# Kernel tuning notes

Hardware: AMD Instinct MI355X
Metric: run time of the kernel (lower is better)

Reference implementation:

```python
import jax, jax.numpy as jnp
import numpy as np

H = 256
T = 2048
B = 64


def setup_inputs() -> dict:
    key = jax.random.key(0)
    ks = jax.random.split(key, 10)
    s = 1.0 / np.sqrt(H)
    return {
        "x": jax.random.normal(ks[0], (T, B, H), dtype=jnp.float32),
        # AttentionLayer params
        "W_b": jax.random.normal(ks[1], (H, H), dtype=jnp.float32) * s,
        "b_b": jnp.zeros((H,), dtype=jnp.float32),
        "v_b": jax.random.normal(ks[2], (1, H), dtype=jnp.float32) * s,
        "W_e": jax.random.normal(ks[3], (H, 2 * H), dtype=jnp.float32) * s,
        "b_e": jnp.zeros((H,), dtype=jnp.float32),
        # LSTMCell params (PyTorch layout: [4H, H], gate order i,f,g,o)
        "W_ih": jax.random.uniform(ks[4], (4 * H, H), dtype=jnp.float32, minval=-s, maxval=s),
        "W_hh": jax.random.uniform(ks[5], (4 * H, H), dtype=jnp.float32, minval=-s, maxval=s),
        "b_ih": jax.random.uniform(ks[6], (4 * H,), dtype=jnp.float32, minval=-s, maxval=s),
        "b_hh": jax.random.uniform(ks[7], (4 * H,), dtype=jnp.float32, minval=-s, maxval=s),
    }


def reference(x, W_b, b_b, v_b, W_e, b_e, W_ih, W_hh, b_ih, b_hh):
    # x: [T, B, H]. Effective recurrence per timestep (inner per-sample loop in
    # the original is dead code: its output writes are overwritten and its
    # states start from zeros each iteration).
    def step(carry, xi):
        h, c = carry  # [B, H] each
        hc = jnp.concatenate([h, c], axis=1)  # [B, 2H]
        a = hc @ W_e.T + b_e                  # [B, H]
        b = xi @ W_b.T + b_b                  # [B, H]
        j = jnp.tanh(a + b) @ v_b.T           # [B, 1]
        w = jax.nn.softmax(j, axis=0) * xi    # softmax over batch dim, [B, H]
        gates = w @ W_ih.T + b_ih + h @ W_hh.T + b_hh  # [B, 4H]
        i_g, f_g, g_g, o_g = jnp.split(gates, 4, axis=1)
        c_new = jax.nn.sigmoid(f_g) * c + jax.nn.sigmoid(i_g) * jnp.tanh(g_g)
        h_new = jax.nn.sigmoid(o_g) * jnp.tanh(c_new)
        return (h_new, c_new), h_new

    Bn, Hn = x.shape[1], x.shape[2]
    init = (jnp.zeros((Bn, Hn), x.dtype), jnp.zeros((Bn, Hn), x.dtype))
    _, output = jax.lax.scan(step, init, x)  # [T, B, H]
    return output
```

## Files before the change

kernel.cpp:

```cpp
#include <hip/hip_runtime.h>
#include <math.h>

constexpr int H   = 256;
constexpr int B   = 64;
constexpr int T   = 2048;
constexpr int G   = 64;
constexpr int NTH = 512;
constexpr int HB  = H * B;

struct SharedMain {
    float wU[256][16];
    float wV[256][16];
    float wA[768][4];
    float U[64][17];
    float V[64][17];
    float ap[64][5];
    alignas(16) float outst[64][4];
    float jp[8][64];
    float bg[16];
    float ba[4];
    float v4[4];
    float s[64];
};
union SharedAll {
    SharedMain m;
    float tile[64][65];
};

__device__ __forceinline__ float sigmoidf_(float v) {
    return 1.0f / (1.0f + expf(-v));
}

__device__ __forceinline__ void grid_barrier(unsigned* bar, unsigned target) {
    __syncthreads();
    if (threadIdx.x == 0) {
        __threadfence();
        __hip_atomic_fetch_add(bar, 1u, __ATOMIC_ACQ_REL, __HIP_MEMORY_SCOPE_AGENT);
        while (__hip_atomic_load(bar, __ATOMIC_ACQUIRE, __HIP_MEMORY_SCOPE_AGENT) < target) {
            __builtin_amdgcn_s_sleep(1);
        }
        __threadfence();
    }
    __syncthreads();
}

__global__ void __launch_bounds__(NTH, 1)
scan_kernel(const float* __restrict__ x,
            const float* __restrict__ W_b,  const float* __restrict__ b_b,
            const float* __restrict__ v_b,  const float* __restrict__ W_e,
            const float* __restrict__ b_e,  const float* __restrict__ W_ih,
            const float* __restrict__ W_hh, const float* __restrict__ b_ih,
            const float* __restrict__ b_hh,
            float* __restrict__ out, float* __restrict__ wsf,
            unsigned* __restrict__ bar)
{
    __shared__ SharedAll sh;
    const int tid = threadIdx.x;
    const int g   = blockIdx.x;

    float* pJ = wsf + 64;
    float* hT = pJ + G * 64;
    float* cT = hT + HB;
    float* xT = out;

    for (int tl = g; tl < T * 4; tl += G) {
        const int t  = tl >> 2;
        const int kc = (tl & 3) << 6;
        __syncthreads();
        for (int q = tid; q < 1024; q += NTH) {
            const int r  = q >> 4;
            const int c4 = (q & 15) << 2;
            const float4 v = *(const float4*)(x + (size_t)t * HB + (size_t)r * H + kc + c4);
            sh.tile[r][c4 + 0] = v.x; sh.tile[r][c4 + 1] = v.y;
            sh.tile[r][c4 + 2] = v.z; sh.tile[r][c4 + 3] = v.w;
        }
        __syncthreads();
        for (int q = tid; q < 1024; q += NTH) {
            const int k  = q >> 4;
            const int b4 = (q & 15) << 2;
            float4 v;
            v.x = sh.tile[b4 + 0][k]; v.y = sh.tile[b4 + 1][k];
            v.z = sh.tile[b4 + 2][k]; v.w = sh.tile[b4 + 3][k];
            *(float4*)(xT + (size_t)t * HB + (size_t)(kc + k) * B + b4) = v;
        }
    }
    __syncthreads();

    for (int e = tid; e < 256 * 16; e += NTH) {
        const int k  = e >> 4;
        const int cl = e & 15;
        const int gate = cl >> 2, oi = cl & 3;
        const int row = gate * H + 4 * g + oi;
        sh.m.wU[k][cl] = W_ih[(size_t)row * H + k];
        sh.m.wV[k][cl] = W_hh[(size_t)row * H + k];
    }
    for (int e = tid; e < 768 * 4; e += NTH) {
        const int r = e >> 2;
        const int i = e & 3;
        const int col = 4 * g + i;
        float w;
        if (r < 512) w = W_e[(size_t)col * 512 + r];
        else         w = W_b[(size_t)col * 256 + (r - 512)];
        sh.m.wA[r][i] = w;
    }
    if (tid < 16) {
        const int gate = tid >> 2, oi = tid & 3;
        const int col = gate * H + 4 * g + oi;
        sh.m.bg[tid] = b_ih[col] + b_hh[col];
    }
    if (tid < 4) {
        sh.m.ba[tid] = b_e[4 * g + tid] + b_b[4 * g + tid];
        sh.m.v4[tid] = v_b[4 * g + tid];
    }
    hT[g * NTH + tid] = 0.0f;

    unsigned nb = 0;
    ++nb; grid_barrier(bar, nb * (unsigned)G);

    const int wv = tid >> 6;
    const int b  = tid & 63;

    for (int t = 0; t < T; ++t) {
        for (int e = tid; e < 64 * 17; e += NTH) { (&sh.m.U[0][0])[e] = 0.0f; (&sh.m.V[0][0])[e] = 0.0f; }
        for (int e = tid; e < 64 * 5; e += NTH) (&sh.m.ap[0][0])[e] = 0.0f;
        __syncthreads();

        if (wv < 4) {
            const int krow = wv << 6;
            const float* src = xT + (size_t)t * HB + (size_t)krow * B;
            float aU[16], aA[4];
            #pragma unroll
            for (int c = 0; c < 16; ++c) aU[c] = 0.0f;
            aA[0] = aA[1] = aA[2] = aA[3] = 0.0f;
            #pragma unroll 4
            for (int kk = 0; kk < 64; ++kk) {
                const float xv = src[kk * B + b];
                const float* wr = sh.m.wU[krow + kk];
                #pragma unroll
                for (int c = 0; c < 16; ++c) aU[c] = fmaf(xv, wr[c], aU[c]);
                const float* wa = sh.m.wA[512 + krow + kk];
                #pragma unroll
                for (int i = 0; i < 4; ++i) aA[i] = fmaf(xv, wa[i], aA[i]);
            }
            #pragma unroll
            for (int c = 0; c < 16; ++c) atomicAdd(&sh.m.U[b][c], aU[c]);
            #pragma unroll
            for (int i = 0; i < 4; ++i) atomicAdd(&sh.m.ap[b][i], aA[i]);
        } else {
            const int krow = (wv - 4) << 6;
            const float* sH = hT + (size_t)krow * B;
            const float* sC = cT + (size_t)krow * B;
            float aV[16], aA[4];
            #pragma unroll
            for (int c = 0; c < 16; ++c) aV[c] = 0.0f;
            aA[0] = aA[1] = aA[2] = aA[3] = 0.0f;
            #pragma unroll 4
            for (int kk = 0; kk < 64; ++kk) {
                const float hv = sH[kk * B + b];
                const float cv = sC[kk * B + b];
                const float* wr = sh.m.wV[krow + kk];
                #pragma unroll
                for (int c = 0; c < 16; ++c) aV[c] = fmaf(hv, wr[c], aV[c]);
                const float* waH = sh.m.wA[krow + kk];
                const float* waC = sh.m.wA[256 + krow + kk];
                #pragma unroll
                for (int i = 0; i < 4; ++i) aA[i] = fmaf(hv, waH[i], fmaf(cv, waC[i], aA[i]));
            }
            #pragma unroll
            for (int c = 0; c < 16; ++c) atomicAdd(&sh.m.V[b][c], aV[c]);
            #pragma unroll
            for (int i = 0; i < 4; ++i) atomicAdd(&sh.m.ap[b][i], aA[i]);
        }
        __syncthreads();

        if (tid < 64) {
            float pj = 0.0f;
            #pragma unroll
            for (int i = 0; i < 4; ++i)
                pj += tanhf(sh.m.ap[tid][i] + sh.m.ba[i]) * sh.m.v4[i];
            pJ[g * 64 + tid] = pj;
        }
        ++nb; grid_barrier(bar, nb * (unsigned)G);

        {
            float jpart = 0.0f;
            const int base = wv * 8;
            #pragma unroll
            for (int gg = 0; gg < 8; ++gg) jpart += pJ[(base + gg) * 64 + b];
            sh.m.jp[wv][b] = jpart;
        }
        __syncthreads();
        if (tid < 64) {
            float jv = 0.0f;
            #pragma unroll
            for (int w = 0; w < 8; ++w) jv += sh.m.jp[w][tid];
            float mx = jv;
            #pragma unroll
            for (int off = 32; off; off >>= 1) mx = fmaxf(mx, __shfl_xor(mx, off));
            const float e = expf(jv - mx);
            float ssum = e;
            #pragma unroll
            for (int off = 32; off; off >>= 1) ssum += __shfl_xor(ssum, off);
            sh.m.s[tid] = e / ssum;
        }
        __syncthreads();

        if (tid < 256) {
            const int oi = tid >> 6;
            const int bb = tid & 63;
            const float sb = sh.m.s[bb];
            const float pI = fmaf(sb, sh.m.U[bb][0  + oi], sh.m.V[bb][0  + oi]) + sh.m.bg[0  + oi];
            const float pF = fmaf(sb, sh.m.U[bb][4  + oi], sh.m.V[bb][4  + oi]) + sh.m.bg[4  + oi];
            const float pG = fmaf(sb, sh.m.U[bb][8  + oi], sh.m.V[bb][8  + oi]) + sh.m.bg[8  + oi];
            const float pO = fmaf(sb, sh.m.U[bb][12 + oi], sh.m.V[bb][12 + oi]) + sh.m.bg[12 + oi];
            const int col = 4 * g + oi;
            const float cold = cT[col * B + bb];
            const float cnew = sigmoidf_(pF) * cold + sigmoidf_(pI) * tanhf(pG);
            const float hnew = sigmoidf_(pO) * tanhf(cnew);
            cT[col * B + bb] = cnew;
            hT[col * B + bb] = hnew;
            sh.m.outst[bb][oi] = hnew;
        }
        __syncthreads();
        if (tid < 64) {
            const float4 v = *(const float4*)sh.m.outst[tid];
            *(float4*)(out + (size_t)t * HB + (size_t)tid * H + 4 * g) = v;
        }
        ++nb; grid_barrier(bar, nb * (unsigned)G);
    }
}

extern "C" void kernel_launch(void* const* d_in, const int* in_sizes, int n_in,
                              void* d_out, int out_size, void* d_ws, size_t ws_size,
                              hipStream_t stream) {
    const float* x    = (const float*)d_in[0];
    const float* W_b  = (const float*)d_in[1];
    const float* b_b  = (const float*)d_in[2];
    const float* v_b  = (const float*)d_in[3];
    const float* W_e  = (const float*)d_in[4];
    const float* b_e  = (const float*)d_in[5];
    const float* W_ih = (const float*)d_in[6];
    const float* W_hh = (const float*)d_in[7];
    const float* b_ih = (const float*)d_in[8];
    const float* b_hh = (const float*)d_in[9];
    float*    out = (float*)d_out;
    float*    wsf = (float*)d_ws;
    unsigned* bar = (unsigned*)d_ws;

    hipMemsetAsync(d_ws, 0, 256, stream);

    void* args[] = { &x, &W_b, &b_b, &v_b, &W_e, &b_e, &W_ih, &W_hh, &b_ih, &b_hh,
                     &out, &wsf, &bar };
    hipLaunchCooperativeKernel((void*)scan_kernel, dim3(G), dim3(NTH), args, 0, stream);
}
```

Baseline: 89.99 ms.

## Replace grid barriers with split arrive/wait counters and double-buffered partials

Replaces the two full grid barriers per timestep with separate arrive/wait counters: one for the attention-score partials, which are now double-buffered by step parity, and one for h/c readiness. The h/c wait is deferred until after each block's x-projection, so that independent work overlaps other blocks' progress. Both the x-projection and the h/c-projection phases are now spread over all 8 waves instead of 4 each. Barrier fences are relaxed to explicit release/acquire fences. The aim is to cut the grid-synchronisation latency that dominates this latency-bound recurrence, at the cost of more delicate memory-ordering reasoning.

```diff
diff --git a/kernel.cpp b/kernel.cpp
--- a/kernel.cpp
+++ b/kernel.cpp
@@ -7,6 +7,7 @@
 constexpr int G   = 64;
 constexpr int NTH = 512;
 constexpr int HB  = H * B;
+constexpr int W   = 2;
 
 struct SharedMain {
     float wU[256][16];
@@ -31,17 +32,17 @@
     return 1.0f / (1.0f + expf(-v));
 }
 
-__device__ __forceinline__ void grid_barrier(unsigned* bar, unsigned target) {
-    __syncthreads();
-    if (threadIdx.x == 0) {
-        __threadfence();
-        __hip_atomic_fetch_add(bar, 1u, __ATOMIC_ACQ_REL, __HIP_MEMORY_SCOPE_AGENT);
-        while (__hip_atomic_load(bar, __ATOMIC_ACQUIRE, __HIP_MEMORY_SCOPE_AGENT) < target) {
-            __builtin_amdgcn_s_sleep(1);
-        }
-        __threadfence();
-    }
-    __syncthreads();
+__device__ __forceinline__ void fence_rel() { __builtin_amdgcn_fence(__ATOMIC_RELEASE, "agent"); }
+__device__ __forceinline__ void fence_acq() { __builtin_amdgcn_fence(__ATOMIC_ACQUIRE, "agent"); }
+
+__device__ __forceinline__ void arrive(unsigned* c) {
+    fence_rel();
+    __hip_atomic_fetch_add(c, 1u, __ATOMIC_RELAXED, __HIP_MEMORY_SCOPE_AGENT);
+}
+__device__ __forceinline__ void wait_for(unsigned* c, unsigned target) {
+    while (__hip_atomic_load(c, __ATOMIC_RELAXED, __HIP_MEMORY_SCOPE_AGENT) < target)
+        __builtin_amdgcn_s_sleep(1);
+    fence_acq();
 }
 
 __global__ void __launch_bounds__(NTH, 1)
@@ -51,15 +52,21 @@
             const float* __restrict__ b_e,  const float* __restrict__ W_ih,
             const float* __restrict__ W_hh, const float* __restrict__ b_ih,
             const float* __restrict__ b_hh,
-            float* __restrict__ out, float* __restrict__ wsf,
-            unsigned* __restrict__ bar)
+            float* __restrict__ out, float* __restrict__ wsf)
 {
     __shared__ SharedAll sh;
     const int tid = threadIdx.x;
     const int g   = blockIdx.x;
 
-    float* pJ = wsf + 64;
-    float* hT = pJ + G * 64;
+    unsigned* cnt = (unsigned*)wsf;
+    unsigned* bar = cnt + 0;
+    unsigned* dj0 = cnt + 16;
+    unsigned* dj1 = cnt + 32;
+    unsigned* dh0 = cnt + 48;
+    unsigned* dh1 = cnt + 64;
+
+    float* pJ = wsf + 128;
+    float* hT = pJ + W * G * 64;
     float* cT = hT + HB;
     float* xT = out;
 
@@ -114,31 +121,37 @@
     }
     hT[g * NTH + tid] = 0.0f;
 
-    unsigned nb = 0;
-    ++nb; grid_barrier(bar, nb * (unsigned)G);
+    __threadfence_block();
+    __syncthreads();
+    if (tid == 0) { arrive(bar); wait_for(bar, (unsigned)G); }
+    __syncthreads();
 
     const int wv = tid >> 6;
     const int b  = tid & 63;
 
     for (int t = 0; t < T; ++t) {
+        const int slot = t & 1;
+        unsigned* dj = slot ? dj1 : dj0;
+        const unsigned tgt = (unsigned)G * ((unsigned)(t >> 1) + 1u);
+
         for (int e = tid; e < 64 * 17; e += NTH) { (&sh.m.U[0][0])[e] = 0.0f; (&sh.m.V[0][0])[e] = 0.0f; }
         for (int e = tid; e < 64 * 5; e += NTH) (&sh.m.ap[0][0])[e] = 0.0f;
         __syncthreads();
 
-        if (wv < 4) {
-            const int krow = wv << 6;
-            const float* src = xT + (size_t)t * HB + (size_t)krow * B;
+        {
+            const int kw = wv << 5;
+            const float* src = xT + (size_t)t * HB + (size_t)kw * B;
             float aU[16], aA[4];
             #pragma unroll
             for (int c = 0; c < 16; ++c) aU[c] = 0.0f;
             aA[0] = aA[1] = aA[2] = aA[3] = 0.0f;
             #pragma unroll 4
-            for (int kk = 0; kk < 64; ++kk) {
+            for (int kk = 0; kk < 32; ++kk) {
                 const float xv = src[kk * B + b];
-                const float* wr = sh.m.wU[krow + kk];
+                const float* wr = sh.m.wU[kw + kk];
                 #pragma unroll
                 for (int c = 0; c < 16; ++c) aU[c] = fmaf(xv, wr[c], aU[c]);
-                const float* wa = sh.m.wA[512 + krow + kk];
+                const float* wa = sh.m.wA[512 + kw + kk];
                 #pragma unroll
                 for (int i = 0; i < 4; ++i) aA[i] = fmaf(xv, wa[i], aA[i]);
             }
@@ -146,23 +159,31 @@
             for (int c = 0; c < 16; ++c) atomicAdd(&sh.m.U[b][c], aU[c]);
             #pragma unroll
             for (int i = 0; i < 4; ++i) atomicAdd(&sh.m.ap[b][i], aA[i]);
-        } else {
-            const int krow = (wv - 4) << 6;
-            const float* sH = hT + (size_t)krow * B;
-            const float* sC = cT + (size_t)krow * B;
+        }
+
+        if (tid == 0 && t > 0) {
+            unsigned* dh = ((t - 1) & 1) ? dh1 : dh0;
+            wait_for(dh, (unsigned)G * ((unsigned)((t - 1) >> 1) + 1u));
+        }
+        __syncthreads();
+
+        {
+            const int kw = wv << 5;
+            const float* sH = hT + (size_t)kw * B;
+            const float* sC = cT + (size_t)kw * B;
             float aV[16], aA[4];
             #pragma unroll
             for (int c = 0; c < 16; ++c) aV[c] = 0.0f;
             aA[0] = aA[1] = aA[2] = aA[3] = 0.0f;
             #pragma unroll 4
-            for (int kk = 0; kk < 64; ++kk) {
+            for (int kk = 0; kk < 32; ++kk) {
                 const float hv = sH[kk * B + b];
                 const float cv = sC[kk * B + b];
-                const float* wr = sh.m.wV[krow + kk];
+                const float* wr = sh.m.wV[kw + kk];
                 #pragma unroll
                 for (int c = 0; c < 16; ++c) aV[c] = fmaf(hv, wr[c], aV[c]);
-                const float* waH = sh.m.wA[krow + kk];
-                const float* waC = sh.m.wA[256 + krow + kk];
+                const float* waH = sh.m.wA[kw + kk];
+                const float* waC = sh.m.wA[256 + kw + kk];
                 #pragma unroll
                 for (int i = 0; i < 4; ++i) aA[i] = fmaf(hv, waH[i], fmaf(cv, waC[i], aA[i]));
             }
@@ -178,15 +199,19 @@
             #pragma unroll
             for (int i = 0; i < 4; ++i)
                 pj += tanhf(sh.m.ap[tid][i] + sh.m.ba[i]) * sh.m.v4[i];
-            pJ[g * 64 + tid] = pj;
-        }
-        ++nb; grid_barrier(bar, nb * (unsigned)G);
+            pJ[(size_t)slot * G * 64 + g * 64 + tid] = pj;
+            __threadfence_block();
+        }
+        __syncthreads();
+        if (tid == 0) { arrive(dj); wait_for(dj, tgt); }
+        __syncthreads();
 
         {
             float jpart = 0.0f;
             const int base = wv * 8;
-            #pragma unroll
-            for (int gg = 0; gg < 8; ++gg) jpart += pJ[(base + gg) * 64 + b];
+            const float* pjs = pJ + (size_t)slot * G * 64;
+            #pragma unroll
+            for (int gg = 0; gg < 8; ++gg) jpart += pjs[(base + gg) * 64 + b];
             sh.m.jp[wv][b] = jpart;
         }
         __syncthreads();
@@ -220,13 +245,15 @@
             cT[col * B + bb] = cnew;
             hT[col * B + bb] = hnew;
             sh.m.outst[bb][oi] = hnew;
-        }
-        __syncthreads();
+            __threadfence_block();
+        }
+        __syncthreads();
+        if (tid == 0) arrive(slot ? dh1 : dh0);
+
         if (tid < 64) {
             const float4 v = *(const float4*)sh.m.outst[tid];
             *(float4*)(out + (size_t)t * HB + (size_t)tid * H + 4 * g) = v;
         }
-        ++nb; grid_barrier(bar, nb * (unsigned)G);
     }
 }
 
@@ -245,11 +272,10 @@
     const float* b_hh = (const float*)d_in[9];
     float*    out = (float*)d_out;
     float*    wsf = (float*)d_ws;
-    unsigned* bar = (unsigned*)d_ws;
-
-    hipMemsetAsync(d_ws, 0, 256, stream);
+
+    hipMemsetAsync(d_ws, 0, 512, stream);
 
     void* args[] = { &x, &W_b, &b_b, &v_b, &W_e, &b_e, &W_ih, &W_hh, &b_ih, &b_hh,
-                     &out, &wsf, &bar };
+                     &out, &wsf };
     hipLaunchCooperativeKernel((void*)scan_kernel, dim3(G), dim3(NTH), args, 0, stream);
 }
```

After: 102.5 ms. 13.9% more time.
